# Kernel optimization log

Measured on AMD Instinct MI355X. Metric: run time of the kernel, lower is better.

The kernel has to match this reference:

```python
import jax, jax.numpy as jnp
import numpy as np

N_ATOMS = 10000
N_STRUCT = 100
N_PSEUDO = 4
N_SPECIES = 4
NMAX = 8
LMAX = 3
HIDDEN = 256
Q = NMAX * N_PSEUDO            # 32 radial*pseudo channels per l
N_FEAT = (LMAX + 1) * Q * Q    # 4096


def setup_inputs() -> dict:
    key = jax.random.key(0)
    ks = jax.random.split(key, 12)
    inp = {}
    for l in range(LMAX + 1):
        inp[f"c{l}"] = jax.random.normal(ks[l], (N_ATOMS, 2 * l + 1, Q), dtype=jnp.float32)
    inp["species_idx"] = jax.random.randint(ks[4], (N_ATOMS,), 0, N_SPECIES, dtype=jnp.int32)
    inp["structure_ids"] = jnp.sort(jax.random.randint(ks[5], (N_ATOMS,), 0, N_STRUCT, dtype=jnp.int32))
    inp["comb_W"] = jax.random.normal(ks[6], (N_PSEUDO, N_SPECIES), dtype=jnp.float32) / np.sqrt(N_SPECIES).astype(np.float32)
    inp["W0"] = jax.random.normal(ks[7], (N_PSEUDO, N_FEAT, HIDDEN), dtype=jnp.float32) / np.sqrt(N_FEAT).astype(np.float32)
    inp["W1"] = jax.random.normal(ks[8], (N_PSEUDO, HIDDEN, HIDDEN), dtype=jnp.float32) / np.sqrt(HIDDEN).astype(np.float32)
    inp["W2"] = jax.random.normal(ks[9], (N_PSEUDO, HIDDEN, 1), dtype=jnp.float32) / np.sqrt(HIDDEN).astype(np.float32)
    return inp


def _power_spectrum(cs):
    # Per-atom outer-product contraction over m, per angular order l.
    feats = []
    for l, c in enumerate(cs):  # c: [A, 2l+1, Q]
        cg = np.float32(1.0 / np.sqrt(2 * l + 1))
        ps = cg * jnp.einsum('amq,amr->aqr', c, c)  # [A, Q, Q]
        feats.append(ps.reshape(c.shape[0], -1))
    return jnp.concatenate(feats, axis=-1)  # [A, N_FEAT]


def reference(c0, c1, c2, c3, species_idx, structure_ids, comb_W, W0, W1, W2):
    features = _power_spectrum([c0, c1, c2, c3])  # [A, F]
    # species-gathered pseudo-species weights: one_hot(a_i) @ combination_matrix
    one_hot = jax.nn.one_hot(species_idx, N_SPECIES, dtype=features.dtype)  # [A, S]
    pw = one_hot @ comb_W.T  # [A, P]
    # embedded_features = features[:, :, None] * pw[:, None, :]
    emb = features[:, None, :] * pw[:, :, None]  # [A, P, F]
    # distinct no-bias MLP per pseudo species (SiLU activations)
    h = jax.nn.silu(jnp.einsum('apf,pfh->aph', emb, W0))
    h = jax.nn.silu(jnp.einsum('aph,phg->apg', h, W1))
    atomic = jnp.einsum('apg,pgo->apo', h, W2)[..., 0].sum(axis=1)  # [A]
    # scatter-sum atomic energies into per-structure totals (index_add_)
    energies = jax.ops.segment_sum(atomic, structure_ids, num_segments=N_STRUCT)
    return energies.reshape(-1, 1)
```

## Files before the change

### kernel.cpp

```cpp
#include <hip/hip_runtime.h>
#include <hip/hip_bf16.h>
#include <cstdint>
#include <cstddef>

#define N_ATOMS 10000
#define NSTRUCT 100
#define NP 4
#define NS 4
#define NF2 2560
#define HID 256
#define APAD 10240

#define PB_FEAT  2500
#define PB_W0    (PB_FEAT + 2560)
#define PB_W1    (PB_W0 + 256)
#define PB_ZERO  (PB_W1 + 300)
#define PB_TOTAL (PB_ZERO + 1)

typedef __attribute__((ext_vector_type(8))) _Float16 f16x8;
typedef __attribute__((ext_vector_type(8))) ushort u16x8;
typedef __attribute__((ext_vector_type(4))) float f32x4;

__device__ __forceinline__ float silu(float x) {
  return x / (1.f + __expf(-x));
}
__device__ __forceinline__ ushort f2h(float x) {
  _Float16 h = (_Float16)x;
  return *reinterpret_cast<ushort*>(&h);
}
__device__ __forceinline__ void cdec(int c, int& q, int& b) {
  if (c < 32)      { q = c >> 2; b = c & 3; }
  else if (c < 56) { int x = c - 32; int j = (x * 171) >> 9; q = 8 + j; b = 1 + (x - j * 3); }
  else if (c < 72) { int x = c - 56; q = 16 + (x >> 1); b = 2 + (x & 1); }
  else             { q = 24 + (c - 72); b = 3; }
}

typedef __attribute__((address_space(3))) uint32_t lds_u32;
typedef const __attribute__((address_space(1))) uint32_t glb_u32;
__device__ __forceinline__ void glds16(const ushort* g, ushort* l) {
  __builtin_amdgcn_global_load_lds((glb_u32*)g, (lds_u32*)l, 16, 0, 0);
}

__global__ __launch_bounds__(256) void prep_kernel(
    const float* __restrict__ c0, const float* __restrict__ c1,
    const float* __restrict__ c2, const float* __restrict__ c3,
    const float* __restrict__ W0, const float* __restrict__ W1,
    ushort* __restrict__ fh, ushort* __restrict__ W0t,
    ushort* __restrict__ W1t, float* __restrict__ out) {
  __shared__ float shbuf[2048];
  int b = blockIdx.x;
  int tid = threadIdx.x;

  if (b < PB_FEAT) {
    int wv = tid >> 6, lane = tid & 63;
    int a = b * 4 + wv;
    float* cs = shbuf + wv * 512;
    for (int i = 0; i < 8; ++i) {
      int e = lane + i * 64;
      float v;
      if (e < 32)       v = c0[a * 32  + e];
      else if (e < 128) v = c1[a * 96  + (e - 32)];
      else if (e < 288) v = c2[a * 160 + (e - 128)];
      else              v = c3[a * 224 + (e - 288)];
      cs[e] = v;
    }
    __syncthreads();
    const float cg[4]  = {1.0f, 0.5773502691896258f, 0.4472135954999579f, 0.3779644730092272f};
    const int  off[4]  = {0, 32, 128, 288};
    const int  nm[4]   = {1, 3, 5, 7};
#pragma unroll
    for (int t = 0; t < 5; ++t) {
      int cc = lane + t * 64;
      int l = cc / 80, c = cc - l * 80;
      int q, bb; cdec(c, q, bb);
      int rb = bb * 8;
      const float* base = cs + off[l];
      float s[8] = {0.f, 0.f, 0.f, 0.f, 0.f, 0.f, 0.f, 0.f};
      for (int m = 0; m < nm[l]; ++m) {
        float bq = base[m * 32 + q];
        float4 v0 = *reinterpret_cast<const float4*>(&base[m * 32 + rb]);
        float4 v1 = *reinterpret_cast<const float4*>(&base[m * 32 + rb + 4]);
        s[0] += bq * v0.x; s[1] += bq * v0.y; s[2] += bq * v0.z; s[3] += bq * v0.w;
        s[4] += bq * v1.x; s[5] += bq * v1.y; s[6] += bq * v1.z; s[7] += bq * v1.w;
      }
      u16x8 o;
#pragma unroll
      for (int u = 0; u < 8; ++u) o[u] = f2h(s[u] * cg[l]);
      *reinterpret_cast<u16x8*>(&fh[(size_t)a * NF2 + cc * 8]) = o;
    }
  } else if (b < PB_W0) {
    int idx = b - PB_FEAT;
    int nx = idx & 7;
    int rest = idx >> 3;
    int ky = rest % 80, p = rest / 80;
    int kt = ky * 32, nt = nx * 32;
    int lx = tid & 31, ly = tid >> 5;
    float (*t)[33] = (float(*)[33])shbuf;
    const float* src = W0 + (size_t)p * 4096 * HID;
#pragma unroll
    for (int i = 0; i < 4; ++i) {
      int kf = kt + ly + i * 8;
      int l = kf / 640, w = kf - l * 640;
      int c = w >> 3, s = w & 7;
      int q, bb; cdec(c, q, bb);
      int r = bb * 8 + s;
      float v = 0.f;
      if (r >= q) {
        v = src[(size_t)(l * 1024 + q * 32 + r) * HID + nt + lx];
        if (r > q) v += src[(size_t)(l * 1024 + r * 32 + q) * HID + nt + lx];
      }
      t[ly + i * 8][lx] = v;
    }
    __syncthreads();
    ushort* dst = W0t + (size_t)p * HID * NF2;
#pragma unroll
    for (int i = 0; i < 4; ++i)
      dst[(size_t)(nt + ly + i * 8) * NF2 + kt + lx] = f2h(t[lx][ly + i * 8]);
  } else if (b < PB_W1) {
    int idx = b - PB_W0;
    int nx = idx & 7, ky = (idx >> 3) & 7, p = idx >> 6;
    int kt = ky * 32, nt = nx * 32;
    int lx = tid & 31, ly = tid >> 5;
    float (*t)[33] = (float(*)[33])shbuf;
    const float* src = W1 + (size_t)p * HID * HID;
#pragma unroll
    for (int i = 0; i < 4; ++i)
      t[ly + i * 8][lx] = src[(size_t)(kt + ly + i * 8) * HID + nt + lx];
    __syncthreads();
    ushort* dst = W1t + (size_t)p * HID * HID;
#pragma unroll
    for (int i = 0; i < 4; ++i)
      dst[(size_t)(nt + ly + i * 8) * HID + kt + lx] = f2h(t[lx][ly + i * 8]);
  } else if (b < PB_ZERO) {
    int idx = b - PB_W1;
    size_t e = (size_t)idx * 2048 + tid * 8;
    u16x8 z = (u16x8){0, 0, 0, 0, 0, 0, 0, 0};
    *reinterpret_cast<u16x8*>(&fh[(size_t)N_ATOMS * NF2 + e]) = z;
  } else {
    if (tid < NSTRUCT) out[tid] = 0.f;
  }
}

__global__ __launch_bounds__(256) void gemm0_mfma(
    const ushort* __restrict__ fh, const ushort* __restrict__ W0t,
    const float* __restrict__ combW, const int* __restrict__ species,
    ushort* __restrict__ h0f) {
  __shared__ ushort As[64 * 64];
  __shared__ ushort Bs[64 * 64];
  int tid = threadIdx.x;
  int linear = blockIdx.y * 8 + blockIdx.x;
  int xc = linear & 7, sq = linear >> 3;
  int bm = ((sq >> 3) * 8 + xc) * 128;
  int bn = (sq & 7) * 128;
  int wid = tid >> 6, lane = tid & 63;
  int wm = (wid >> 1) * 64, wn = (wid & 1) * 64;
  int mh = wid >> 1, nh = wid & 1;

  int pr = tid >> 3, pc = tid & 7;
  int lg = pc ^ (pr & 7);
  int mhalf = lg >> 2, kc = lg & 3;
  const ushort* gaA1 = fh  + ((size_t)(bm + pr + 64 * mhalf) * NF2 + kc * 8);
  const ushort* gaA2 = gaA1 + (size_t)32 * NF2;
  const ushort* gaB1 = W0t + ((size_t)(bn + pr + 64 * mhalf) * NF2 + kc * 8);
  const ushort* gaB2 = gaB1 + (size_t)32 * NF2;
  ushort* lA = As + tid * 8;
  ushort* lB = Bs + tid * 8;

  f32x4 acc[4][4];
#pragma unroll
  for (int i = 0; i < 4; ++i)
#pragma unroll
    for (int j = 0; j < 4; ++j) acc[i][j] = (f32x4){0.f, 0.f, 0.f, 0.f};

  int mrow = lane & 15;
  int h7 = mrow & 7;
  int qv = lane >> 4;
  int pcA = ((mh << 2) | qv) ^ h7;
  int pcB = ((nh << 2) | qv) ^ h7;

  for (int k0 = 0; k0 < NF2; k0 += 32) {
    glds16(gaA1 + k0, lA);
    glds16(gaA2 + k0, lA + 2048);
    glds16(gaB1 + k0, lB);
    glds16(gaB2 + k0, lB + 2048);
    __syncthreads();

    f16x8 af[4], bf[4];
#pragma unroll
    for (int i = 0; i < 4; ++i) {
      af[i] = *reinterpret_cast<const f16x8*>(&As[(i * 16 + mrow) * 64 + pcA * 8]);
      bf[i] = *reinterpret_cast<const f16x8*>(&Bs[(i * 16 + mrow) * 64 + pcB * 8]);
    }
#pragma unroll
    for (int i = 0; i < 4; ++i)
#pragma unroll
      for (int j = 0; j < 4; ++j)
        acc[i][j] = __builtin_amdgcn_mfma_f32_16x16x32_f16(af[i], bf[j], acc[i][j], 0, 0, 0);
    __syncthreads();
  }

  int p = bn >> 8;
  int col = lane & 15, rbase = (lane >> 4) * 4;
#pragma unroll
  for (int i = 0; i < 4; ++i) {
#pragma unroll
    for (int r = 0; r < 4; ++r) {
      int m = bm + wm + i * 16 + rbase + r;
      bool live = (m < N_ATOMS);
      float pw = live ? combW[p * NS + species[m]] : 0.f;
#pragma unroll
      for (int j = 0; j < 4; ++j) {
        int n = bn + wn + j * 16 + col;
        float v = live ? silu(pw * acc[i][j][r]) : 0.f;
        h0f[(size_t)m * 1024 + n] = f2h(v);
      }
    }
  }
}

__global__ __launch_bounds__(256) void mlp1_mfma(
    const ushort* __restrict__ h0f, const ushort* __restrict__ W1t,
    const float* __restrict__ W2, const int* __restrict__ sid,
    float* __restrict__ out) {
  __shared__ ushort As[64 * 256];
  __shared__ float sout[NSTRUCT];
  int tid = threadIdx.x;
  int linear = blockIdx.x;
  int xc = linear & 7, s = linear >> 3;
  int p = s & 3, t = s >> 2;
  int bm = ((t >> 1) * 8 + xc) * 128 + (t & 1) * 64;
  int wid = tid >> 6, lane = tid & 63;
  int wn = wid * 64;

  if (tid < NSTRUCT) sout[tid] = 0.f;

  int mrow = lane & 15;
  int qv = lane >> 4;
  int h7 = mrow & 7;

#pragma unroll
  for (int s8 = 0; s8 < 8; ++s8) {
    int d = s8 * 256 + tid;
    int r = d >> 5, pcs = d & 31;
    int lc = pcs ^ (r & 7);
    glds16(h0f + (size_t)(bm + r) * 1024 + p * 256 + lc * 8, As + d * 8);
  }

  const ushort* wb = W1t + (size_t)p * HID * HID;
  f16x8 breg[4][8];
#pragma unroll
  for (int j = 0; j < 4; ++j) {
    const ushort* row = wb + (size_t)(wn + j * 16 + mrow) * 256 + qv * 8;
#pragma unroll
    for (int ki = 0; ki < 8; ++ki)
      breg[j][ki] = *reinterpret_cast<const f16x8*>(row + ki * 32);
  }

  __syncthreads();

  f32x4 acc[4][4];
#pragma unroll
  for (int i = 0; i < 4; ++i)
#pragma unroll
    for (int j = 0; j < 4; ++j) acc[i][j] = (f32x4){0.f, 0.f, 0.f, 0.f};

#pragma unroll
  for (int ki = 0; ki < 8; ++ki) {
    f16x8 af[4];
#pragma unroll
    for (int i = 0; i < 4; ++i) {
      int row = i * 16 + mrow;
      int pc2 = (ki * 4 + qv) ^ h7;
      af[i] = *reinterpret_cast<const f16x8*>(&As[row * 256 + pc2 * 8]);
    }
#pragma unroll
    for (int i = 0; i < 4; ++i)
#pragma unroll
      for (int j = 0; j < 4; ++j)
        acc[i][j] = __builtin_amdgcn_mfma_f32_16x16x32_f16(af[i], breg[j][ki], acc[i][j], 0, 0, 0);
  }

  int col = lane & 15, quad = lane >> 4;
  float w2j[4];
#pragma unroll
  for (int j = 0; j < 4; ++j) w2j[j] = W2[p * 256 + wn + j * 16 + col];
#pragma unroll
  for (int i = 0; i < 4; ++i) {
#pragma unroll
    for (int r = 0; r < 4; ++r) {
      float v = silu(acc[i][0][r]) * w2j[0] + silu(acc[i][1][r]) * w2j[1]
              + silu(acc[i][2][r]) * w2j[2] + silu(acc[i][3][r]) * w2j[3];
      v += __shfl_xor(v, 1, 64);
      v += __shfl_xor(v, 2, 64);
      v += __shfl_xor(v, 4, 64);
      v += __shfl_xor(v, 8, 64);
      if (col == 0) {
        int m = bm + i * 16 + quad * 4 + r;
        if (m < N_ATOMS) atomicAdd(&sout[sid[m]], v);
      }
    }
  }
  __syncthreads();
  if (tid < NSTRUCT) {
    float v = sout[tid];
    if (v != 0.f) atomicAdd(&out[tid], v);
  }
}

extern "C" void kernel_launch(void* const* d_in, const int* in_sizes, int n_in,
                              void* d_out, int out_size, void* d_ws, size_t ws_size,
                              hipStream_t stream) {
  const float* c0      = (const float*)d_in[0];
  const float* c1      = (const float*)d_in[1];
  const float* c2      = (const float*)d_in[2];
  const float* c3      = (const float*)d_in[3];
  const int*   species = (const int*)d_in[4];
  const int*   sid     = (const int*)d_in[5];
  const float* combW   = (const float*)d_in[6];
  const float* W0      = (const float*)d_in[7];
  const float* W1      = (const float*)d_in[8];
  const float* W2      = (const float*)d_in[9];
  float*       out     = (float*)d_out;

  ushort* fh  = (ushort*)d_ws;
  ushort* W0t = fh  + (size_t)APAD * NF2;
  ushort* W1t = W0t + (size_t)NP * HID * NF2;
  ushort* h0f = W1t + (size_t)NP * HID * HID;

  prep_kernel<<<PB_TOTAL, 256, 0, stream>>>(c0, c1, c2, c3, W0, W1,
                                            fh, W0t, W1t, out);

  dim3 g2(8, APAD / 128);
  gemm0_mfma<<<g2, 256, 0, stream>>>(fh, W0t, combW, species, h0f);

  mlp1_mfma<<<640, 256, 0, stream>>>(h0f, W1t, W2, sid, out);
}
```

Before: 205.1 us.

## Double-buffer LDS tiles and deepen K-step to 64 in gemm0 MFMA kernel

The first-layer GEMM now keeps two LDS buffers and issues global-to-LDS loads for the next K tile while MFMAs run on the current one, replacing the single-buffer load-sync-compute loop. Each K step doubles from 32 to 64, which halves the number of barriers and uses a new swizzled tile layout. The cost is four times as much shared memory (64 KB per block), which can lower occupancy. The loop also relies on the single trailing barrier to order async LDS writes against reads of the other buffer.

```diff
diff --git a/kernel.cpp b/kernel.cpp
--- a/kernel.cpp
+++ b/kernel.cpp
@@ -145,8 +145,7 @@
     const ushort* __restrict__ fh, const ushort* __restrict__ W0t,
     const float* __restrict__ combW, const int* __restrict__ species,
     ushort* __restrict__ h0f) {
-  __shared__ ushort As[64 * 64];
-  __shared__ ushort Bs[64 * 64];
+  __shared__ ushort sh[32768];
   int tid = threadIdx.x;
   int linear = blockIdx.y * 8 + blockIdx.x;
   int xc = linear & 7, sq = linear >> 3;
@@ -154,17 +153,19 @@
   int bn = (sq & 7) * 128;
   int wid = tid >> 6, lane = tid & 63;
   int wm = (wid >> 1) * 64, wn = (wid & 1) * 64;
-  int mh = wid >> 1, nh = wid & 1;
-
-  int pr = tid >> 3, pc = tid & 7;
-  int lg = pc ^ (pr & 7);
-  int mhalf = lg >> 2, kc = lg & 3;
-  const ushort* gaA1 = fh  + ((size_t)(bm + pr + 64 * mhalf) * NF2 + kc * 8);
-  const ushort* gaA2 = gaA1 + (size_t)32 * NF2;
-  const ushort* gaB1 = W0t + ((size_t)(bn + pr + 64 * mhalf) * NF2 + kc * 8);
-  const ushort* gaB2 = gaB1 + (size_t)32 * NF2;
-  ushort* lA = As + tid * 8;
-  ushort* lB = Bs + tid * 8;
+
+  const ushort* srcA[4];
+  const ushort* srcB[4];
+  int ldsu[4];
+#pragma unroll
+  for (int j = 0; j < 4; ++j) {
+    int u = j * 256 + tid;
+    int r = u >> 3;
+    int lc = (u & 7) ^ (r & 7);
+    srcA[j] = fh  + (size_t)(bm + r) * NF2 + lc * 8;
+    srcB[j] = W0t + (size_t)(bn + r) * NF2 + lc * 8;
+    ldsu[j] = u * 8;
+  }
 
   f32x4 acc[4][4];
 #pragma unroll
@@ -173,29 +174,46 @@
     for (int j = 0; j < 4; ++j) acc[i][j] = (f32x4){0.f, 0.f, 0.f, 0.f};
 
   int mrow = lane & 15;
+  int qv = lane >> 4;
   int h7 = mrow & 7;
-  int qv = lane >> 4;
-  int pcA = ((mh << 2) | qv) ^ h7;
-  int pcB = ((nh << 2) | qv) ^ h7;
-
-  for (int k0 = 0; k0 < NF2; k0 += 32) {
-    glds16(gaA1 + k0, lA);
-    glds16(gaA2 + k0, lA + 2048);
-    glds16(gaB1 + k0, lB);
-    glds16(gaB2 + k0, lB + 2048);
-    __syncthreads();
-
-    f16x8 af[4], bf[4];
-#pragma unroll
-    for (int i = 0; i < 4; ++i) {
-      af[i] = *reinterpret_cast<const f16x8*>(&As[(i * 16 + mrow) * 64 + pcA * 8]);
-      bf[i] = *reinterpret_cast<const f16x8*>(&Bs[(i * 16 + mrow) * 64 + pcB * 8]);
-    }
-#pragma unroll
-    for (int i = 0; i < 4; ++i)
-#pragma unroll
-      for (int j = 0; j < 4; ++j)
-        acc[i][j] = __builtin_amdgcn_mfma_f32_16x16x32_f16(af[i], bf[j], acc[i][j], 0, 0, 0);
+  int pc0 = (qv ^ h7) * 8;
+
+#pragma unroll
+  for (int j = 0; j < 4; ++j) {
+    glds16(srcA[j], sh + ldsu[j]);
+    glds16(srcB[j], sh + 8192 + ldsu[j]);
+  }
+  __syncthreads();
+
+  const int NK = NF2 / 64;
+  for (int t = 0; t < NK; ++t) {
+    int cur = (t & 1) << 14;
+    int nxt = 16384 - cur;
+    if (t + 1 < NK) {
+      int k0 = (t + 1) * 64;
+#pragma unroll
+      for (int j = 0; j < 4; ++j) {
+        glds16(srcA[j] + k0, sh + nxt + ldsu[j]);
+        glds16(srcB[j] + k0, sh + nxt + 8192 + ldsu[j]);
+      }
+    }
+    const ushort* As = sh + cur;
+    const ushort* Bs = sh + cur + 8192;
+#pragma unroll
+    for (int h = 0; h < 2; ++h) {
+      int pc = pc0 ^ (h << 5);
+      f16x8 af[4], bf[4];
+#pragma unroll
+      for (int i = 0; i < 4; ++i) {
+        af[i] = *reinterpret_cast<const f16x8*>(&As[(wm + i * 16 + mrow) * 64 + pc]);
+        bf[i] = *reinterpret_cast<const f16x8*>(&Bs[(wn + i * 16 + mrow) * 64 + pc]);
+      }
+#pragma unroll
+      for (int i = 0; i < 4; ++i)
+#pragma unroll
+        for (int j = 0; j < 4; ++j)
+          acc[i][j] = __builtin_amdgcn_mfma_f32_16x16x32_f16(af[i], bf[j], acc[i][j], 0, 0, 0);
+    }
     __syncthreads();
   }
 
```

New measurement: 218.4 us. +6.5%, slower.

## Double-buffer LDS tiles in gemm0 with async global-to-LDS prefetch

Applied to the files above, without the earlier changes.

The gemm0 kernel's LDS tile storage becomes two buffers, and the loads for the next-but-one k-step are issued while MFMAs run on the current one. Explicit vmcnt and lgkmcnt waits, raw barriers and inline ds_read_b128 replace the two __syncthreads per iteration. The goal is to hide global-load latency behind the matrix math. In exchange, LDS per block doubles, which may lower occupancy. The hand-written waitcnt logic is also fragile and could race if the counts are wrong.

```diff
diff --git a/kernel.cpp b/kernel.cpp
--- a/kernel.cpp
+++ b/kernel.cpp
@@ -36,9 +36,15 @@
 }
 
 typedef __attribute__((address_space(3))) uint32_t lds_u32;
+typedef __attribute__((address_space(3))) ushort lds_ushort;
 typedef const __attribute__((address_space(1))) uint32_t glb_u32;
 __device__ __forceinline__ void glds16(const ushort* g, ushort* l) {
   __builtin_amdgcn_global_load_lds((glb_u32*)g, (lds_u32*)l, 16, 0, 0);
+}
+__device__ __forceinline__ f16x8 dsr(uint32_t addr) {
+  f16x8 r;
+  asm volatile("ds_read_b128 %0, %1" : "=v"(r) : "v"(addr));
+  return r;
 }
 
 __global__ __launch_bounds__(256) void prep_kernel(
@@ -145,8 +151,7 @@
     const ushort* __restrict__ fh, const ushort* __restrict__ W0t,
     const float* __restrict__ combW, const int* __restrict__ species,
     ushort* __restrict__ h0f) {
-  __shared__ ushort As[64 * 64];
-  __shared__ ushort Bs[64 * 64];
+  __shared__ ushort sh[16384];
   int tid = threadIdx.x;
   int linear = blockIdx.y * 8 + blockIdx.x;
   int xc = linear & 7, sq = linear >> 3;
@@ -159,12 +164,18 @@
   int pr = tid >> 3, pc = tid & 7;
   int lg = pc ^ (pr & 7);
   int mhalf = lg >> 2, kc = lg & 3;
-  const ushort* gaA1 = fh  + ((size_t)(bm + pr + 64 * mhalf) * NF2 + kc * 8);
-  const ushort* gaA2 = gaA1 + (size_t)32 * NF2;
-  const ushort* gaB1 = W0t + ((size_t)(bn + pr + 64 * mhalf) * NF2 + kc * 8);
-  const ushort* gaB2 = gaB1 + (size_t)32 * NF2;
-  ushort* lA = As + tid * 8;
-  ushort* lB = Bs + tid * 8;
+  const ushort* gA1 = fh  + ((size_t)(bm + pr + 64 * mhalf) * NF2 + kc * 8);
+  const ushort* gA2 = gA1 + (size_t)32 * NF2;
+  const ushort* gB1 = W0t + ((size_t)(bn + pr + 64 * mhalf) * NF2 + kc * 8);
+  const ushort* gB2 = gB1 + (size_t)32 * NF2;
+  ushort* l0 = sh + tid * 8;
+
+#define STAGE(B) do {                          \
+    glds16(gA1, l0 + (B) * 8192);              \
+    glds16(gA2, l0 + (B) * 8192 + 2048);       \
+    glds16(gB1, l0 + (B) * 8192 + 4096);       \
+    glds16(gB2, l0 + (B) * 8192 + 6144);       \
+    gA1 += 32; gA2 += 32; gB1 += 32; gB2 += 32; } while (0)
 
   f32x4 acc[4][4];
 #pragma unroll
@@ -172,32 +183,48 @@
 #pragma unroll
     for (int j = 0; j < 4; ++j) acc[i][j] = (f32x4){0.f, 0.f, 0.f, 0.f};
 
-  int mrow = lane & 15;
-  int h7 = mrow & 7;
-  int qv = lane >> 4;
+  int mrow = lane & 15, qv = lane >> 4, h7 = mrow & 7;
   int pcA = ((mh << 2) | qv) ^ h7;
   int pcB = ((nh << 2) | qv) ^ h7;
-
-  for (int k0 = 0; k0 < NF2; k0 += 32) {
-    glds16(gaA1 + k0, lA);
-    glds16(gaA2 + k0, lA + 2048);
-    glds16(gaB1 + k0, lB);
-    glds16(gaB2 + k0, lB + 2048);
-    __syncthreads();
-
+  uint32_t lbase = (uint32_t)(size_t)(lds_ushort*)sh;
+  uint32_t aA[4], aB[4];
+#pragma unroll
+  for (int i = 0; i < 4; ++i) {
+    aA[i] = lbase + 2u * (uint32_t)((i * 16 + mrow) * 64 + pcA * 8);
+    aB[i] = lbase + 2u * (uint32_t)(4096 + (i * 16 + mrow) * 64 + pcB * 8);
+  }
+
+  STAGE(0);
+  STAGE(1);
+  asm volatile("s_waitcnt vmcnt(4)" ::: "memory");
+  __builtin_amdgcn_s_barrier();
+
+  const int NK = NF2 / 32;
+  for (int t = 0; t < NK; ++t) {
+    uint32_t bb = (uint32_t)(t & 1) * 16384u;
     f16x8 af[4], bf[4];
 #pragma unroll
     for (int i = 0; i < 4; ++i) {
-      af[i] = *reinterpret_cast<const f16x8*>(&As[(i * 16 + mrow) * 64 + pcA * 8]);
-      bf[i] = *reinterpret_cast<const f16x8*>(&Bs[(i * 16 + mrow) * 64 + pcB * 8]);
-    }
+      af[i] = dsr(aA[i] + bb);
+      bf[i] = dsr(aB[i] + bb);
+    }
+    asm volatile("s_waitcnt lgkmcnt(0)" ::: "memory");
+    __builtin_amdgcn_sched_barrier(0);
 #pragma unroll
     for (int i = 0; i < 4; ++i)
 #pragma unroll
       for (int j = 0; j < 4; ++j)
         acc[i][j] = __builtin_amdgcn_mfma_f32_16x16x32_f16(af[i], bf[j], acc[i][j], 0, 0, 0);
-    __syncthreads();
-  }
+    __builtin_amdgcn_s_barrier();
+    if (t < NK - 2) {
+      STAGE(t & 1);
+      asm volatile("s_waitcnt vmcnt(4)" ::: "memory");
+    } else {
+      asm volatile("s_waitcnt vmcnt(0)" ::: "memory");
+    }
+    __builtin_amdgcn_s_barrier();
+  }
+#undef STAGE
 
   int p = bn >> 8;
   int col = lane & 15, rbase = (lane >> 4) * 4;
```

Measured after the change: 210.0 us. 2.4% more time.
